# Optimization experiments

Measured on AMD Instinct MI355X. Metric: run time of the kernel, lower is better.

## Reference

```python
import jax, jax.numpy as jnp
import numpy as np

SUB_NO, T_NO, T_DATA, E_NO, I_NO, N_BASIS = 20, 200, 50000, 2000, 500, 20


def _make_cos_basis():
    x = np.arange(T_NO, dtype=np.float32)
    raw = 6.0 * np.log(x + 1.0)  # cos_scale=6, cos_shift=1
    basis = np.zeros((N_BASIS, T_NO), np.float32)
    for i in range(N_BASIS):
        phi = 0.5 * np.pi * i
        b = 0.5 * np.cos(raw - phi) + 0.5
        basis[i] = np.where((raw < phi - np.pi) | (raw > phi + np.pi), 0.0, b)
    return basis


def _make_tree():
    C = np.zeros((SUB_NO, SUB_NO), np.int32)
    for p in range(SUB_NO):
        for c in (2 * p + 1, 2 * p + 2):
            if c < SUB_NO:
                C[p, c] = 1
    return C


def _one_hot_assign(n_syn):
    C = np.zeros((SUB_NO, n_syn), np.int32)
    C[np.arange(n_syn) % SUB_NO, np.arange(n_syn)] = 1
    return C


def setup_inputs() -> dict:
    key = jax.random.key(0)
    ks = jax.random.split(key, 12)
    f32 = jnp.float32
    S_e = (jax.random.uniform(ks[0], (T_DATA, E_NO)) < 0.02).astype(f32)
    S_i = (jax.random.uniform(ks[1], (T_DATA, I_NO)) < 0.02).astype(f32)
    Z = (jax.random.uniform(ks[2], (T_DATA,)) < 0.05).astype(f32)
    return {
        "S_e": S_e, "S_i": S_i, "Z": Z,
        "C_den": jnp.asarray(_make_tree()),
        "C_syn_e": jnp.asarray(_one_hot_assign(E_NO)),
        "C_syn_i": jnp.asarray(_one_hot_assign(I_NO)),
        "cos_basis": jnp.asarray(_make_cos_basis()),
        "W_syn": jax.random.normal(ks[3], (SUB_NO, N_BASIS, 2), f32) * 0.1,
        "W_hist": jax.random.normal(ks[4], (N_BASIS,), f32) * 0.1,
        "W_sub": jnp.ones((SUB_NO,), f32) * 0.1,
        "W_spk": jnp.ones((1,), f32),
        "Tau_spk": jnp.ones((1,), f32) * 3.0,
        "V_o": jax.random.normal(ks[5], (1,), f32),
        "Theta": jax.random.normal(ks[6], (SUB_NO,), f32) * 0.1,
        "weight1": jax.random.normal(ks[7], (SUB_NO, 5), f32) * 0.1,
        "weight2": jax.random.normal(ks[8], (SUB_NO, 5, 5), f32) * 0.1,
        "weight3": jax.random.normal(ks[9], (SUB_NO, 5, 5), f32) * 0.1,
        "weight4": jax.random.normal(ks[10], (5, SUB_NO), f32) * 0.1,
    }


def reference(S_e, S_i, Z, C_den, C_syn_e, C_syn_i, cos_basis, W_syn, W_hist,
              W_sub, W_spk, Tau_spk, V_o, Theta, weight1, weight2, weight3, weight4):
    f32 = jnp.float32
    T = S_e.shape[0]
    sub_no = weight1.shape[0]
    T_no = cos_basis.shape[1]
    Cd = C_den.astype(f32)

    # synapse -> subunit projection
    syn_e = S_e @ C_syn_e.astype(f32).T  # [T, sub]
    syn_i = S_i @ C_syn_i.astype(f32).T

    e_kern = W_syn[:, :, 0] @ cos_basis  # [sub, T_no]
    i_kern = W_syn[:, :, 1] @ cos_basis

    def grouped_causal_conv(x, kern):
        # torch: pad T_no-1 zeros in front, grouped conv with flipped kernel (true causal conv)
        xp = jnp.pad(x, ((T_no - 1, 0), (0, 0))).T[None]  # [1, sub, T+T_no-1]
        k = kern[:, None, ::-1]  # [sub, 1, T_no]
        y = jax.lax.conv_general_dilated(xp, k, (1,), 'VALID',
                                         dimension_numbers=('NCH', 'OIH', 'NCH'),
                                         feature_group_count=x.shape[1])
        return y[0].T  # [T, sub]

    syn = grouped_causal_conv(syn_e, e_kern) + grouped_causal_conv(syn_i, i_kern)

    def causal_conv_lag1(z, kern):
        # torch: pad T_no zeros in front, valid conv with flipped kernel, drop last -> [T]
        zp = jnp.pad(z, (T_no, 0))[None, None]  # [1,1,T+T_no]
        k = kern[None, None, ::-1]
        y = jax.lax.conv_general_dilated(zp, k, (1,), 'VALID',
                                         dimension_numbers=('NCH', 'OIH', 'NCH'))
        return y[0, 0, :-1]

    hist_kern = W_hist @ cos_basis  # [T_no]
    hist_filt = causal_conv_lag1(Z, hist_kern)

    lrelu = jax.nn.leaky_relu  # negative_slope 0.01 matches torch default
    W_sub2 = W_sub ** 2

    def sub_mlp(s, x):
        h = lrelu(x[:, None] * weight1[s][None, :])  # [T,5]
        h = lrelu(h @ weight2[s])
        h = lrelu(h @ weight3[s])
        return h @ weight4[:, s]  # [T]

    # tree recurrence: children have higher index, processed last-to-first
    ns_out = jnp.zeros((T, sub_no), f32)
    for s in range(sub_no - 1):
        sub_idx = sub_no - 1 - s
        agg = ns_out @ (Cd[sub_idx] * W_sub2)  # equals gather-leaf weighted sum (0 if leaf)
        ns_in = lrelu(syn[:, sub_idx] + Theta[sub_idx] + agg)
        ns_out = ns_out.at[:, sub_idx].set(sub_mlp(sub_idx, ns_in))

    root_in = lrelu(hist_filt + syn[:, 0] + ns_out @ (Cd[0] * W_sub2) + Theta[0])
    final_Z = jax.nn.sigmoid(sub_mlp(0, root_in))

    t = jnp.arange(T_no, dtype=f32)
    t_tau = t / Tau_spk[0] ** 2
    spk_kern = t_tau * jnp.exp(-t_tau) * W_spk[0] ** 2
    final_V = causal_conv_lag1(Z, spk_kern) + V_o[0]

    out_filters = jnp.concatenate([e_kern, i_kern, hist_kern[None, :]], axis=0)
    return final_V, final_Z, out_filters
```

## Files before the change

### kernel.cpp

```cpp
#include <hip/hip_runtime.h>
#include <math.h>

#define T_DATA 50000
#define SUB_NO 20
#define T_NO 200
#define N_BASIS 20

#define WS_E    0
#define WS_I    1000000
#define WS_EKT  2000000
#define WS_IKT  2004000
#define WS_HS   2008000
#define WS_WSE  2008400

__device__ __forceinline__ float lrelu(float x) { return x > 0.f ? x : 0.01f * x; }

__global__ __launch_bounds__(256) void k1_reduce(const float* __restrict__ Se,
                                                 const float* __restrict__ Si,
                                                 float* __restrict__ ws) {
    int gid = blockIdx.x * 256 + threadIdx.x;
    if (gid >= T_DATA * 5) return;
    int t = gid / 5, sg = gid % 5;
    const float4* Se4 = (const float4*)Se;
    const float4* Si4 = (const float4*)Si;

    float4 a = make_float4(0.f, 0.f, 0.f, 0.f);
    int base_e = t * 500 + sg;
    #pragma unroll 4
    for (int g = 0; g < 100; g++) {
        float4 v = Se4[base_e + g * 5];
        a.x += v.x; a.y += v.y; a.z += v.z; a.w += v.w;
    }
    float4 b = make_float4(0.f, 0.f, 0.f, 0.f);
    int base_i = t * 125 + sg;
    #pragma unroll
    for (int g = 0; g < 25; g++) {
        float4 v = Si4[base_i + g * 5];
        b.x += v.x; b.y += v.y; b.z += v.z; b.w += v.w;
    }
    ((float4*)(ws + WS_E))[t * 5 + sg] = a;
    ((float4*)(ws + WS_I))[t * 5 + sg] = b;
}

__global__ __launch_bounds__(256) void k2_small(const int* __restrict__ C_den,
                                                const float* __restrict__ cb,
                                                const float* __restrict__ W_syn,
                                                const float* __restrict__ W_hist,
                                                const float* __restrict__ W_sub,
                                                const float* __restrict__ W_spk,
                                                const float* __restrict__ Tau,
                                                float* __restrict__ ws,
                                                float* __restrict__ out) {
    int tid = threadIdx.x;
    for (int j = tid; j < 4000; j += 256) {
        int s = j / 200, tau = j % 200;
        float se = 0.f, si = 0.f;
        #pragma unroll
        for (int b = 0; b < N_BASIS; b++) {
            float c = cb[b * 200 + tau];
            se += W_syn[(s * N_BASIS + b) * 2 + 0] * c;
            si += W_syn[(s * N_BASIS + b) * 2 + 1] * c;
        }
        ws[WS_EKT + tau * 20 + s] = se;
        ws[WS_IKT + tau * 20 + s] = si;
        out[2 * T_DATA + j] = se;
        out[2 * T_DATA + 4000 + j] = si;
    }
    for (int j = tid; j < 200; j += 256) {
        float h = 0.f;
        #pragma unroll
        for (int b = 0; b < N_BASIS; b++) h += W_hist[b] * cb[b * 200 + j];
        out[2 * T_DATA + 8000 + j] = h;
        float tau2 = Tau[0] * Tau[0];
        float tt = (float)j / tau2;
        float sk = tt * expf(-tt) * W_spk[0] * W_spk[0];
        ws[WS_HS + 2 * j + 0] = h;
        ws[WS_HS + 2 * j + 1] = sk;
    }
    for (int j = tid; j < 400; j += 256) {
        int c = j % 20;
        ws[WS_WSE + j] = (float)C_den[j] * W_sub[c] * W_sub[c];
    }
}

__device__ __forceinline__ float sub_mlp(int s, float x,
                                         const float* __restrict__ w1,
                                         const float* __restrict__ w2,
                                         const float* __restrict__ w3,
                                         const float* __restrict__ w4) {
    float h1[5], h2[5], h3[5];
    #pragma unroll
    for (int k = 0; k < 5; k++) h1[k] = lrelu(x * w1[s * 5 + k]);
    #pragma unroll
    for (int j = 0; j < 5; j++) {
        float v = 0.f;
        #pragma unroll
        for (int k = 0; k < 5; k++) v += h1[k] * w2[s * 25 + k * 5 + j];
        h2[j] = lrelu(v);
    }
    #pragma unroll
    for (int j = 0; j < 5; j++) {
        float v = 0.f;
        #pragma unroll
        for (int k = 0; k < 5; k++) v += h2[k] * w3[s * 25 + k * 5 + j];
        h3[j] = lrelu(v);
    }
    float o = 0.f;
    #pragma unroll
    for (int k = 0; k < 5; k++) o += h3[k] * w4[k * 20 + s];
    return o;
}

#define K3_BLK 128
#define K3_ROWS (K3_BLK + 199)

__global__ __launch_bounds__(128) void k3_main(const float* __restrict__ ws,
                                               const float* __restrict__ Z,
                                               const float* __restrict__ Theta,
                                               const float* __restrict__ w1,
                                               const float* __restrict__ w2,
                                               const float* __restrict__ w3,
                                               const float* __restrict__ w4,
                                               const float* __restrict__ Vo,
                                               float* __restrict__ out) {
    __shared__ float4 lds_e4[K3_ROWS * 5];
    __shared__ float4 lds_i4[K3_ROWS * 5];
    __shared__ float  lds_z[K3_ROWS + 1];
    int tid = threadIdx.x;
    int t0 = blockIdx.x * K3_BLK;

    long base = (long)(t0 - 199) * 20;
    const float4* wsE4 = (const float4*)(ws + WS_E);
    const float4* wsI4 = (const float4*)(ws + WS_I);
    for (int f4 = tid; f4 < K3_ROWS * 5; f4 += K3_BLK) {
        long g = base + (long)f4 * 4;
        float4 ve = make_float4(0.f, 0.f, 0.f, 0.f);
        float4 vi = ve;
        if (g >= 0 && g < (long)T_DATA * 20) {
            ve = wsE4[g >> 2];
            vi = wsI4[g >> 2];
        }
        lds_e4[f4] = ve;
        lds_i4[f4] = vi;
    }
    for (int f = tid; f < K3_ROWS + 1; f += K3_BLK) {
        int u = t0 - 200 + f;
        lds_z[f] = (u >= 0 && u < T_DATA) ? Z[u] : 0.f;
    }
    __syncthreads();

    const float* lds_e = (const float*)lds_e4;
    const float* lds_i = (const float*)lds_i4;
    const float4* ekT = (const float4*)(ws + WS_EKT);
    const float4* ikT = (const float4*)(ws + WS_IKT);
    const float2* hs  = (const float2*)(ws + WS_HS);

    float acc[20];
    #pragma unroll
    for (int s = 0; s < 20; s++) acc[s] = 0.f;
    float ha = 0.f, sa = 0.f;

    for (int tau = 0; tau < T_NO; tau++) {
        int r = tid + 199 - tau;
        const float4* le = (const float4*)&lds_e[r * 20];
        const float4* li = (const float4*)&lds_i[r * 20];
        float zv = lds_z[r];
        float2 hv = hs[tau];
        ha += zv * hv.x;
        sa += zv * hv.y;
        #pragma unroll
        for (int sg = 0; sg < 5; sg++) {
            float4 e4 = le[sg], i4 = li[sg];
            float4 ke = ekT[tau * 5 + sg], ki = ikT[tau * 5 + sg];
            acc[sg * 4 + 0] += e4.x * ke.x + i4.x * ki.x;
            acc[sg * 4 + 1] += e4.y * ke.y + i4.y * ki.y;
            acc[sg * 4 + 2] += e4.z * ke.z + i4.z * ki.z;
            acc[sg * 4 + 3] += e4.w * ke.w + i4.w * ki.w;
        }
    }

    int t = t0 + tid;
    if (t >= T_DATA) return;

    const float* wse = ws + WS_WSE;
    float ns[20];
    #pragma unroll
    for (int s = 0; s < 20; s++) ns[s] = 0.f;
    #pragma unroll
    for (int si = 19; si >= 1; si--) {
        float ag = 0.f;
        #pragma unroll
        for (int c = 0; c < 20; c++) ag += wse[si * 20 + c] * ns[c];
        float x = lrelu(acc[si] + Theta[si] + ag);
        ns[si] = sub_mlp(si, x, w1, w2, w3, w4);
    }
    float ag0 = 0.f;
    #pragma unroll
    for (int c = 0; c < 20; c++) ag0 += wse[c] * ns[c];
    float x0 = lrelu(ha + acc[0] + ag0 + Theta[0]);
    float zf = sub_mlp(0, x0, w1, w2, w3, w4);

    out[t] = sa + Vo[0];
    out[T_DATA + t] = 1.f / (1.f + expf(-zf));
}

extern "C" void kernel_launch(void* const* d_in, const int* in_sizes, int n_in,
                              void* d_out, int out_size, void* d_ws, size_t ws_size,
                              hipStream_t stream) {
    const float* S_e    = (const float*)d_in[0];
    const float* S_i    = (const float*)d_in[1];
    const float* Z      = (const float*)d_in[2];
    const int*   C_den  = (const int*)d_in[3];
    const float* cb     = (const float*)d_in[6];
    const float* W_syn  = (const float*)d_in[7];
    const float* W_hist = (const float*)d_in[8];
    const float* W_sub  = (const float*)d_in[9];
    const float* W_spk  = (const float*)d_in[10];
    const float* Tau    = (const float*)d_in[11];
    const float* V_o    = (const float*)d_in[12];
    const float* Theta  = (const float*)d_in[13];
    const float* w1     = (const float*)d_in[14];
    const float* w2     = (const float*)d_in[15];
    const float* w3     = (const float*)d_in[16];
    const float* w4     = (const float*)d_in[17];
    float* out = (float*)d_out;
    float* ws  = (float*)d_ws;

    k1_reduce<<<(T_DATA * 5 + 255) / 256, 256, 0, stream>>>(S_e, S_i, ws);
    k2_small<<<1, 256, 0, stream>>>(C_den, cb, W_syn, W_hist, W_sub, W_spk, Tau, ws, out);
    k3_main<<<(T_DATA + K3_BLK - 1) / K3_BLK, K3_BLK, 0, stream>>>(
        ws, Z, Theta, w1, w2, w3, w4, V_o, out);
}
```

Measured before the change: 732.1 us.

## Split convolution across subunit-group threads and move history filter to separate kernel

```diff
diff --git a/kernel.cpp b/kernel.cpp
--- a/kernel.cpp
+++ b/kernel.cpp
@@ -12,6 +12,7 @@
 #define WS_IKT  2004000
 #define WS_HS   2008000
 #define WS_WSE  2008400
+#define WS_HF   2008800
 
 __device__ __forceinline__ float lrelu(float x) { return x > 0.f ? x : 0.01f * x; }
 
@@ -83,6 +84,36 @@
     }
 }
 
+#define KH_BLK 128
+#define KH_R 327
+__global__ __launch_bounds__(KH_BLK) void kh_hist(const float* __restrict__ Z,
+                                                  const float* __restrict__ ws,
+                                                  const float* __restrict__ Vo,
+                                                  float* __restrict__ out,
+                                                  float* __restrict__ wsw) {
+    __shared__ float z[KH_R];
+    int x = threadIdx.x;
+    int t0 = blockIdx.x * KH_BLK;
+    for (int f = x; f < KH_R; f += KH_BLK) {
+        int u = t0 - 200 + f;
+        z[f] = (u >= 0 && u < T_DATA) ? Z[u] : 0.f;
+    }
+    __syncthreads();
+    const float2* hs = (const float2*)(ws + WS_HS);
+    float ha = 0.f, sa = 0.f;
+    for (int tau = 0; tau < T_NO; tau++) {
+        float zv = z[x + 199 - tau];
+        float2 hv = hs[tau];
+        ha += zv * hv.x;
+        sa += zv * hv.y;
+    }
+    int t = t0 + x;
+    if (t < T_DATA) {
+        out[t] = sa + Vo[0];
+        wsw[WS_HF + t] = ha;
+    }
+}
+
 __device__ __forceinline__ float sub_mlp(int s, float x,
                                          const float* __restrict__ w1,
                                          const float* __restrict__ w2,
@@ -111,97 +142,101 @@
     return o;
 }
 
-#define K3_BLK 128
-#define K3_ROWS (K3_BLK + 199)
-
-__global__ __launch_bounds__(128) void k3_main(const float* __restrict__ ws,
-                                               const float* __restrict__ Z,
+#define K3_X 64
+#define K3_T 128
+#define K3_R (K3_T + 199)
+#define K3_RP 328
+
+__global__ __launch_bounds__(320) void k3_main(const float* __restrict__ ws,
                                                const float* __restrict__ Theta,
                                                const float* __restrict__ w1,
                                                const float* __restrict__ w2,
                                                const float* __restrict__ w3,
                                                const float* __restrict__ w4,
-                                               const float* __restrict__ Vo,
                                                float* __restrict__ out) {
-    __shared__ float4 lds_e4[K3_ROWS * 5];
-    __shared__ float4 lds_i4[K3_ROWS * 5];
-    __shared__ float  lds_z[K3_ROWS + 1];
-    int tid = threadIdx.x;
-    int t0 = blockIdx.x * K3_BLK;
-
-    long base = (long)(t0 - 199) * 20;
+    __shared__ float4 tile[2][5][K3_RP];
+    int x = threadIdx.x;
+    int sg = threadIdx.y;
+    int t0 = blockIdx.x * K3_T;
+
     const float4* wsE4 = (const float4*)(ws + WS_E);
     const float4* wsI4 = (const float4*)(ws + WS_I);
-    for (int f4 = tid; f4 < K3_ROWS * 5; f4 += K3_BLK) {
-        long g = base + (long)f4 * 4;
+    int lin = x + 64 * sg;
+    long gbase = (long)(t0 - 199) * 5;
+    for (int f = lin; f < K3_R * 5; f += 320) {
+        long g = gbase + f;
+        int row = f / 5, gg = f % 5;
         float4 ve = make_float4(0.f, 0.f, 0.f, 0.f);
         float4 vi = ve;
-        if (g >= 0 && g < (long)T_DATA * 20) {
-            ve = wsE4[g >> 2];
-            vi = wsI4[g >> 2];
+        if (g >= 0 && g < (long)T_DATA * 5) {
+            ve = wsE4[g];
+            vi = wsI4[g];
         }
-        lds_e4[f4] = ve;
-        lds_i4[f4] = vi;
-    }
-    for (int f = tid; f < K3_ROWS + 1; f += K3_BLK) {
-        int u = t0 - 200 + f;
-        lds_z[f] = (u >= 0 && u < T_DATA) ? Z[u] : 0.f;
-    }
-    __syncthreads();
-
-    const float* lds_e = (const float*)lds_e4;
-    const float* lds_i = (const float*)lds_i4;
-    const float4* ekT = (const float4*)(ws + WS_EKT);
-    const float4* ikT = (const float4*)(ws + WS_IKT);
-    const float2* hs  = (const float2*)(ws + WS_HS);
-
-    float acc[20];
-    #pragma unroll
-    for (int s = 0; s < 20; s++) acc[s] = 0.f;
-    float ha = 0.f, sa = 0.f;
+        tile[0][gg][row] = ve;
+        tile[1][gg][row] = vi;
+    }
+    __syncthreads();
+
+    const float4* eK = (const float4*)(ws + WS_EKT);
+    const float4* iK = (const float4*)(ws + WS_IKT);
+    float4 acc0 = make_float4(0.f, 0.f, 0.f, 0.f);
+    float4 acc1 = acc0;
+    const float4* te = &tile[0][sg][0];
+    const float4* ti = &tile[1][sg][0];
 
     for (int tau = 0; tau < T_NO; tau++) {
-        int r = tid + 199 - tau;
-        const float4* le = (const float4*)&lds_e[r * 20];
-        const float4* li = (const float4*)&lds_i[r * 20];
-        float zv = lds_z[r];
-        float2 hv = hs[tau];
-        ha += zv * hv.x;
-        sa += zv * hv.y;
-        #pragma unroll
-        for (int sg = 0; sg < 5; sg++) {
-            float4 e4 = le[sg], i4 = li[sg];
-            float4 ke = ekT[tau * 5 + sg], ki = ikT[tau * 5 + sg];
-            acc[sg * 4 + 0] += e4.x * ke.x + i4.x * ki.x;
-            acc[sg * 4 + 1] += e4.y * ke.y + i4.y * ki.y;
-            acc[sg * 4 + 2] += e4.z * ke.z + i4.z * ki.z;
-            acc[sg * 4 + 3] += e4.w * ke.w + i4.w * ki.w;
+        float4 ke = eK[tau * 5 + sg];
+        float4 ki = iK[tau * 5 + sg];
+        int r = x + 199 - tau;
+        float4 e0 = te[r],      i0 = ti[r];
+        float4 e1 = te[r + 64], i1 = ti[r + 64];
+        acc0.x += e0.x * ke.x + i0.x * ki.x;
+        acc0.y += e0.y * ke.y + i0.y * ki.y;
+        acc0.z += e0.z * ke.z + i0.z * ki.z;
+        acc0.w += e0.w * ke.w + i0.w * ki.w;
+        acc1.x += e1.x * ke.x + i1.x * ki.x;
+        acc1.y += e1.y * ke.y + i1.y * ki.y;
+        acc1.z += e1.z * ke.z + i1.z * ki.z;
+        acc1.w += e1.w * ke.w + i1.w * ki.w;
+    }
+
+    __syncthreads();
+    float* accL = (float*)&tile[0][0][0];
+    accL[x * 20 + sg * 4 + 0] = acc0.x;
+    accL[x * 20 + sg * 4 + 1] = acc0.y;
+    accL[x * 20 + sg * 4 + 2] = acc0.z;
+    accL[x * 20 + sg * 4 + 3] = acc0.w;
+    accL[(x + 64) * 20 + sg * 4 + 0] = acc1.x;
+    accL[(x + 64) * 20 + sg * 4 + 1] = acc1.y;
+    accL[(x + 64) * 20 + sg * 4 + 2] = acc1.z;
+    accL[(x + 64) * 20 + sg * 4 + 3] = acc1.w;
+    __syncthreads();
+
+    if (sg != 0) return;
+    const float* wse = ws + WS_WSE;
+    #pragma unroll
+    for (int half = 0; half < 2; half++) {
+        int t = t0 + x + half * 64;
+        if (t >= T_DATA) break;
+        const float* acc = &accL[(x + half * 64) * 20];
+        float ns[20];
+        #pragma unroll
+        for (int s = 0; s < 20; s++) ns[s] = 0.f;
+        #pragma unroll
+        for (int si = 19; si >= 1; si--) {
+            float ag = 0.f;
+            #pragma unroll
+            for (int c = 0; c < 20; c++) ag += wse[si * 20 + c] * ns[c];
+            float xx = lrelu(acc[si] + Theta[si] + ag);
+            ns[si] = sub_mlp(si, xx, w1, w2, w3, w4);
         }
-    }
-
-    int t = t0 + tid;
-    if (t >= T_DATA) return;
-
-    const float* wse = ws + WS_WSE;
-    float ns[20];
-    #pragma unroll
-    for (int s = 0; s < 20; s++) ns[s] = 0.f;
-    #pragma unroll
-    for (int si = 19; si >= 1; si--) {
-        float ag = 0.f;
-        #pragma unroll
-        for (int c = 0; c < 20; c++) ag += wse[si * 20 + c] * ns[c];
-        float x = lrelu(acc[si] + Theta[si] + ag);
-        ns[si] = sub_mlp(si, x, w1, w2, w3, w4);
-    }
-    float ag0 = 0.f;
-    #pragma unroll
-    for (int c = 0; c < 20; c++) ag0 += wse[c] * ns[c];
-    float x0 = lrelu(ha + acc[0] + ag0 + Theta[0]);
-    float zf = sub_mlp(0, x0, w1, w2, w3, w4);
-
-    out[t] = sa + Vo[0];
-    out[T_DATA + t] = 1.f / (1.f + expf(-zf));
+        float ag0 = 0.f;
+        #pragma unroll
+        for (int c = 0; c < 20; c++) ag0 += wse[c] * ns[c];
+        float x0 = lrelu(ws[WS_HF + t] + acc[0] + ag0 + Theta[0]);
+        float zf = sub_mlp(0, x0, w1, w2, w3, w4);
+        out[T_DATA + t] = 1.f / (1.f + expf(-zf));
+    }
 }
 
 extern "C" void kernel_launch(void* const* d_in, const int* in_sizes, int n_in,
@@ -228,6 +263,8 @@
 
     k1_reduce<<<(T_DATA * 5 + 255) / 256, 256, 0, stream>>>(S_e, S_i, ws);
     k2_small<<<1, 256, 0, stream>>>(C_den, cb, W_syn, W_hist, W_sub, W_spk, Tau, ws, out);
-    k3_main<<<(T_DATA + K3_BLK - 1) / K3_BLK, K3_BLK, 0, stream>>>(
-        ws, Z, Theta, w1, w2, w3, w4, V_o, out);
-}
+    kh_hist<<<(T_DATA + KH_BLK - 1) / KH_BLK, KH_BLK, 0, stream>>>(Z, ws, V_o, out, ws);
+    dim3 b3(K3_X, 5);
+    k3_main<<<(T_DATA + K3_T - 1) / K3_T, b3, 0, stream>>>(
+        ws, Theta, w1, w2, w3, w4, out);
+}
```

After: 811.7 us. +10.9%, slower.
